# Kernel tuning notes

Hardware: AMD Instinct MI355X
Metric: run time of the kernel (lower is better)

The kernel has to match this reference:

```python
import jax, jax.numpy as jnp
import numpy as np

S, B, C = 14, 2, 20          # grid size, boxes per cell, classes
LAMBDA_COORD, LAMBDA_NOOBJ = 5.0, 0.5
NCH = 5 * B + C              # 30 channels


def setup_inputs() -> dict:
    key = jax.random.key(0)
    k1, k2, k3 = jax.random.split(key, 3)
    Nb = 4096
    # positive values: loss takes sqrt(w), sqrt(h)
    pred = jax.random.uniform(k1, (Nb, S, S, NCH), dtype=jnp.float32, minval=0.05, maxval=1.0)
    target = jax.random.uniform(k2, (Nb, S, S, NCH), dtype=jnp.float32, minval=0.05, maxval=1.0)
    # binarize conf channels so coord (conf>0) / noobj (conf==0) partition the cells
    objf = (jax.random.uniform(k3, (Nb, S, S)) < 0.3).astype(jnp.float32)
    for b in range(B):
        target = target.at[..., 4 + 5 * b].set(objf)
    return {"pred_tensor": pred, "target_tensor": target}


def _to_xyxy(box):
    # box [..., 5] (or [..., B, 5]): cell-relative x,y and global w,h -> corners
    xy = box[..., :2] / S
    half = 0.5 * box[..., 2:4]
    return jnp.concatenate([xy - half, xy + half], axis=-1)


def reference(pred_tensor, target_tensor):
    pred, target = pred_tensor, target_tensor
    obj = (target[..., 4] > 0).astype(pred.dtype)      # [Nb,S,S]
    noobj = (target[..., 4] == 0).astype(pred.dtype)   # [Nb,S,S]

    pb = pred[..., :5 * B].reshape(pred.shape[:3] + (B, 5))     # [Nb,S,S,B,5]
    tb = target[..., :5 * B].reshape(target.shape[:3] + (B, 5))  # [Nb,S,S,B,5]

    # no-object confidence loss: conf channel of every box slot in noobj cells
    loss_noobj = jnp.sum(noobj[..., None] * (pb[..., 4] - tb[..., 4]) ** 2)

    # IoU of each of B predicted boxes vs the (first) target box of the cell
    pxy = _to_xyxy(pb)                        # [Nb,S,S,B,4]
    txy = _to_xyxy(tb[..., 0, :])[..., None, :]  # [Nb,S,S,1,4]
    lt = jnp.maximum(pxy[..., :2], txy[..., :2])
    rb = jnp.minimum(pxy[..., 2:], txy[..., 2:])
    wh = jnp.clip(rb - lt, 0.0)
    inter = wh[..., 0] * wh[..., 1]           # [Nb,S,S,B]
    area_p = (pxy[..., 2] - pxy[..., 0]) * (pxy[..., 3] - pxy[..., 1])
    area_t = (txy[..., 2] - txy[..., 0]) * (txy[..., 3] - txy[..., 1])
    iou = inter / (area_p + area_t - inter)

    max_iou = jax.lax.stop_gradient(jnp.max(iou, axis=-1))  # torch uses .data (detach)
    r = jnp.argmax(iou, axis=-1)              # responsible box index [Nb,S,S]

    pr = jnp.take_along_axis(pb, r[..., None, None], axis=3)[..., 0, :]  # [Nb,S,S,5]
    tr = jnp.take_along_axis(tb, r[..., None, None], axis=3)[..., 0, :]

    m = obj
    loss_xy = jnp.sum(m[..., None] * (pr[..., :2] - tr[..., :2]) ** 2)
    # guard sqrt in masked-out cells (values there don't matter)
    safe_pwh = jnp.where(m[..., None] > 0, pr[..., 2:4], 1.0)
    safe_twh = jnp.where(m[..., None] > 0, tr[..., 2:4], 1.0)
    loss_wh = jnp.sum(m[..., None] * (jnp.sqrt(safe_pwh) - jnp.sqrt(safe_twh)) ** 2)
    loss_obj = jnp.sum(m * (pr[..., 4] - max_iou) ** 2)
    loss_class = jnp.sum(m[..., None] * (pred[..., 5 * B:] - target[..., 5 * B:]) ** 2)

    loss = LAMBDA_COORD * (loss_xy + loss_wh) + loss_obj + LAMBDA_NOOBJ * loss_noobj + loss_class
    return loss / pred.shape[0]
```

## Files before the change

kernel.cpp:

```cpp
#include <hip/hip_runtime.h>


#define S_GRID 14
#define NB 4096
#define NCELL (NB * S_GRID * S_GRID)
#define NCH 30
#define CELLS_PER_BLOCK 256
#define NBLOCKS (NCELL / CELLS_PER_BLOCK)

__global__ __launch_bounds__(256, 4) void yolo_loss_partial(
    const float* __restrict__ pred, const float* __restrict__ target,
    float* __restrict__ partial)
{
    const int cell = blockIdx.x * CELLS_PER_BLOCK + threadIdx.x;
    const float2* __restrict__ p2 = (const float2*)(pred + (size_t)cell * NCH);
    const float2* __restrict__ t2 = (const float2*)(target + (size_t)cell * NCH);

    float p[10], t[10];
#pragma unroll
    for (int i = 0; i < 5; ++i) {
        float2 a = p2[i]; p[2 * i] = a.x; p[2 * i + 1] = a.y;
        float2 b = t2[i]; t[2 * i] = b.x; t[2 * i + 1] = b.y;
    }

    const float t4 = t[4];
    const bool obj = (t4 > 0.0f);

    float dn0 = p[4] - t[4];
    float dn1 = p[9] - t[9];
    float noobj_l = (t4 == 0.0f) ? (dn0 * dn0 + dn1 * dn1) : 0.0f;

    const float invS = 1.0f / 14.0f;
    float tcx = t[0] * invS, tcy = t[1] * invS;
    float tx1 = tcx - 0.5f * t[2], ty1 = tcy - 0.5f * t[3];
    float tx2 = tcx + 0.5f * t[2], ty2 = tcy + 0.5f * t[3];
    float area_t = (tx2 - tx1) * (ty2 - ty1);

    float iou[2];
#pragma unroll
    for (int b = 0; b < 2; ++b) {
        const float* pb = p + 5 * b;
        float cx = pb[0] * invS, cy = pb[1] * invS;
        float x1 = cx - 0.5f * pb[2], y1 = cy - 0.5f * pb[3];
        float x2 = cx + 0.5f * pb[2], y2 = cy + 0.5f * pb[3];
        float lx = fmaxf(x1, tx1), ly = fmaxf(y1, ty1);
        float rx = fminf(x2, tx2), ry = fminf(y2, ty2);
        float wx = fmaxf(rx - lx, 0.0f), wy = fmaxf(ry - ly, 0.0f);
        float inter = wx * wy;
        float area_p = (x2 - x1) * (y2 - y1);
        iou[b] = inter / (area_p + area_t - inter);
    }

    int r = (iou[1] > iou[0]) ? 1 : 0;
    float max_iou = fmaxf(iou[0], iou[1]);

    float lcls = 0.0f;
#pragma unroll
    for (int i = 5; i < 15; ++i) {
        float2 a = p2[i];
        float2 b = t2[i];
        float d0 = a.x - b.x, d1 = a.y - b.y;
        lcls += d0 * d0 + d1 * d1;
    }

    float obj_l = 0.0f;
    if (obj) {
        const float* pr = p + 5 * r;
        const float* tr = t + 5 * r;
        float dx = pr[0] - tr[0], dy = pr[1] - tr[1];
        float lxy = dx * dx + dy * dy;
        float dw = sqrtf(pr[2]) - sqrtf(tr[2]);
        float dh = sqrtf(pr[3]) - sqrtf(tr[3]);
        float lwh = dw * dw + dh * dh;
        float dob = pr[4] - max_iou;
        float lob = dob * dob;
        obj_l = 5.0f * (lxy + lwh) + lob + lcls;
    }
    float loss = obj_l + 0.5f * noobj_l;

    float v = loss;
#pragma unroll
    for (int off = 32; off > 0; off >>= 1)
        v += __shfl_down(v, off, 64);

    __shared__ float red[4];
    const int lane = threadIdx.x & 63;
    const int wid = threadIdx.x >> 6;
    if (lane == 0) red[wid] = v;
    __syncthreads();
    if (threadIdx.x == 0)
        partial[blockIdx.x] = red[0] + red[1] + red[2] + red[3];
}

__global__ __launch_bounds__(256) void yolo_loss_finalize(
    const float* __restrict__ partial, float* __restrict__ out)
{
    double s = 0.0;
    for (int i = threadIdx.x; i < NBLOCKS; i += 256)
        s += (double)partial[i];

    __shared__ double sh[256];
    sh[threadIdx.x] = s;
    __syncthreads();
#pragma unroll
    for (int step = 128; step > 0; step >>= 1) {
        if (threadIdx.x < step) sh[threadIdx.x] += sh[threadIdx.x + step];
        __syncthreads();
    }
    if (threadIdx.x == 0)
        out[0] = (float)(sh[0] / (double)NB);
}

extern "C" void kernel_launch(void* const* d_in, const int* in_sizes, int n_in,
                              void* d_out, int out_size, void* d_ws, size_t ws_size,
                              hipStream_t stream) {
    const float* pred = (const float*)d_in[0];
    const float* target = (const float*)d_in[1];
    float* out = (float*)d_out;
    float* partial = (float*)d_ws;

    yolo_loss_partial<<<NBLOCKS, 256, 0, stream>>>(pred, target, partial);
    yolo_loss_finalize<<<1, 256, 0, stream>>>(partial, out);
}
```

Measured before the change: 209.5 us.

## Stage cell data through LDS with double-buffered async global-to-LDS copies

Each thread used to read its own cell straight from global memory with a 120-byte stride, which gives poorly coalesced accesses. The kernel now copies contiguous chunks of 128 cells of pred and target into shared memory with 16-byte global_load_lds copies issued by all threads, double-buffered over 8 chunks per block. The per-cell math is then read from LDS by half the threads, and the responsible-box selection becomes selects instead of indexed access. In exchange it uses about 61 KB of LDS per block, which limits how many blocks fit per CU, leaves half the threads idle during compute, and relies on the compiler waiting on the async copies before each barrier.

```diff
diff --git a/kernel.cpp b/kernel.cpp
--- a/kernel.cpp
+++ b/kernel.cpp
@@ -1,20 +1,46 @@
 #include <hip/hip_runtime.h>
 
 
-#define S_GRID 14
 #define NB 4096
-#define NCELL (NB * S_GRID * S_GRID)
+#define NCELL (NB * 14 * 14)
 #define NCH 30
-#define CELLS_PER_BLOCK 256
+#define CHUNK_CELLS 128
+#define CHUNKS_PER_BLOCK 8
+#define CELLS_PER_BLOCK (CHUNK_CELLS * CHUNKS_PER_BLOCK)
 #define NBLOCKS (NCELL / CELLS_PER_BLOCK)
+#define CHUNK_FLOATS (CHUNK_CELLS * NCH)
+#define CHUNK_F4 (CHUNK_FLOATS / 4)
 
-__global__ __launch_bounds__(256, 4) void yolo_loss_partial(
-    const float* __restrict__ pred, const float* __restrict__ target,
-    float* __restrict__ partial)
+#define GLOBAL_AS __attribute__((address_space(1)))
+#define LDS_AS    __attribute__((address_space(3)))
+
+__device__ __forceinline__ void async_copy16(const float* g, float* l) {
+    __builtin_amdgcn_global_load_lds((const GLOBAL_AS void*)g, (LDS_AS void*)l,
+                                     16, 0, 0);
+}
+
+__device__ __forceinline__ void stage_chunk(const float* __restrict__ pred,
+                                            const float* __restrict__ target,
+                                            float* pbuf, float* tbuf,
+                                            size_t cellbase, int tid)
 {
-    const int cell = blockIdx.x * CELLS_PER_BLOCK + threadIdx.x;
-    const float2* __restrict__ p2 = (const float2*)(pred + (size_t)cell * NCH);
-    const float2* __restrict__ t2 = (const float2*)(target + (size_t)cell * NCH);
+    const float* gp = pred + cellbase * NCH;
+    const float* gt = target + cellbase * NCH;
+#pragma unroll
+    for (int r = 0; r < 4; ++r) {
+        int idx = r * 256 + tid;
+        if (idx < CHUNK_F4) {
+            async_copy16(gp + (size_t)idx * 4, pbuf + idx * 4);
+            async_copy16(gt + (size_t)idx * 4, tbuf + idx * 4);
+        }
+    }
+}
+
+__device__ __forceinline__ float cell_loss_lds(const float* __restrict__ pl,
+                                               const float* __restrict__ tl)
+{
+    const float2* p2 = (const float2*)pl;
+    const float2* t2 = (const float2*)tl;
 
     float p[10], t[10];
 #pragma unroll
@@ -51,8 +77,14 @@
         iou[b] = inter / (area_p + area_t - inter);
     }
 
-    int r = (iou[1] > iou[0]) ? 1 : 0;
+    const bool r = (iou[1] > iou[0]);
     float max_iou = fmaxf(iou[0], iou[1]);
+
+    float pr0 = r ? p[5] : p[0], tr0 = r ? t[5] : t[0];
+    float pr1 = r ? p[6] : p[1], tr1 = r ? t[6] : t[1];
+    float pr2 = r ? p[7] : p[2], tr2 = r ? t[7] : t[2];
+    float pr3 = r ? p[8] : p[3], tr3 = r ? t[8] : t[3];
+    float pr4 = r ? p[9] : p[4];
 
     float lcls = 0.0f;
 #pragma unroll
@@ -65,25 +97,48 @@
 
     float obj_l = 0.0f;
     if (obj) {
-        const float* pr = p + 5 * r;
-        const float* tr = t + 5 * r;
-        float dx = pr[0] - tr[0], dy = pr[1] - tr[1];
+        float dx = pr0 - tr0, dy = pr1 - tr1;
         float lxy = dx * dx + dy * dy;
-        float dw = sqrtf(pr[2]) - sqrtf(tr[2]);
-        float dh = sqrtf(pr[3]) - sqrtf(tr[3]);
+        float dw = sqrtf(pr2) - sqrtf(tr2);
+        float dh = sqrtf(pr3) - sqrtf(tr3);
         float lwh = dw * dw + dh * dh;
-        float dob = pr[4] - max_iou;
+        float dob = pr4 - max_iou;
         float lob = dob * dob;
         obj_l = 5.0f * (lxy + lwh) + lob + lcls;
     }
-    float loss = obj_l + 0.5f * noobj_l;
+    return obj_l + 0.5f * noobj_l;
+}
 
-    float v = loss;
+__global__ __launch_bounds__(256) void yolo_loss_partial(
+    const float* __restrict__ pred, const float* __restrict__ target,
+    float* __restrict__ partial)
+{
+    __shared__ __align__(16) float buf[2][2][CHUNK_FLOATS];
+    __shared__ float red[4];
+
+    const int tid = threadIdx.x;
+    const size_t blockcell = (size_t)blockIdx.x * CELLS_PER_BLOCK;
+
+    stage_chunk(pred, target, buf[0][0], buf[0][1], blockcell, tid);
+    __syncthreads();
+
+    float acc = 0.0f;
+    for (int c = 0; c < CHUNKS_PER_BLOCK; ++c) {
+        const int cur = c & 1;
+        if (c + 1 < CHUNKS_PER_BLOCK)
+            stage_chunk(pred, target, buf[cur ^ 1][0], buf[cur ^ 1][1],
+                        blockcell + (size_t)(c + 1) * CHUNK_CELLS, tid);
+        if (tid < CHUNK_CELLS)
+            acc += cell_loss_lds(&buf[cur][0][tid * NCH],
+                                 &buf[cur][1][tid * NCH]);
+        __syncthreads();
+    }
+
+    float v = acc;
 #pragma unroll
     for (int off = 32; off > 0; off >>= 1)
         v += __shfl_down(v, off, 64);
 
-    __shared__ float red[4];
     const int lane = threadIdx.x & 63;
     const int wid = threadIdx.x >> 6;
     if (lane == 0) red[wid] = v;
```

Measured after the change: 214.6 us. 1.02x slower.
